# Kernel optimization log

Measured on AMD Instinct MI355X. Metric: run time of the kernel, lower is better.

## Reference

```python
import jax, jax.numpy as jnp
import numpy as np

B, H, W, L, T = 64, 512, 512, 2048, 8192
DIM = 256


def setup_inputs() -> dict:
    key = jax.random.key(0)
    ks = jax.random.split(key, 16)

    def lin(k, out_f, in_f):
        kw, kb = jax.random.split(k)
        s = 1.0 / np.sqrt(in_f)
        Wt = jax.random.uniform(kw, (out_f, in_f), jnp.float32, -s, s)
        b = jax.random.uniform(kb, (out_f,), jnp.float32, -s, s)
        return Wt, b

    Wv1, bv1 = lin(ks[3], 16, 3)
    Wv2, bv2 = lin(ks[4], 64, 16)
    Wv3, bv3 = lin(ks[5], 256, 64)
    Wa, ba = lin(ks[6], 256, 1)
    Wf, bf = lin(ks[7], 128, 128)
    Wg, bg = lin(ks[8], 128, 128)
    text_emb = jax.random.normal(ks[9], (256, 256), jnp.float32)

    return {
        "vision_ycbcr": jax.random.normal(ks[0], (B, 3, H, W), jnp.float32),
        "audio_wave": jax.random.normal(ks[1], (B, T), jnp.float32),
        "text_bytes": jax.random.randint(ks[2], (B, L), 0, 256),
        "Wv1": Wv1, "bv1": bv1, "Wv2": Wv2, "bv2": bv2,
        "Wv3": Wv3, "bv3": bv3, "text_emb": text_emb,
        "Wa": Wa, "ba": ba, "Wf": Wf, "bf": bf, "Wg": Wg, "bg": bg,
    }


def _forward(vision_ycbcr, audio_wave, text_bytes,
             Wv1, bv1, Wv2, bv2, Wv3, bv3, text_emb, Wa, ba, Wf, bf, Wg, bg):
    # vision: spatial mean -> 3-layer SiLU MLP to 256
    v = vision_ycbcr.mean(axis=(-1, -2))                      # [B,3]
    v = jax.nn.silu(v @ Wv1.T + bv1)                          # [B,16]
    v = jax.nn.silu(v @ Wv2.T + bv2)                          # [B,64]
    v = v @ Wv3.T + bv3                                       # [B,256]

    # text: embedding gather + mean pool
    t = text_emb[text_bytes].mean(axis=1)                     # [B,256]

    # audio: per-sample Linear(1,256) then mean pool (materialized as in torch)
    a = (audio_wave[..., None] * Wa[:, 0] + ba).mean(axis=1)  # [B,256]

    # Pancharatnam-Berry phase (inputs are real, so phase in {0, pi})
    inner_vt = jnp.sum(v * t, axis=-1)
    inner_ta = jnp.sum(t * a, axis=-1)
    inner_av = jnp.sum(a * v, axis=-1)
    gamma = jnp.angle(inner_vt * inner_ta * inner_av)[:, None]  # [B,1]

    combined = (v + t + a) * jnp.cos(gamma)                   # Re[exp(i*gamma)]

    # reversible coupling: y1 = x1 + F(x2); y2 = x2 + G(y1)
    x1, x2 = combined[:, :128], combined[:, 128:]
    y1 = x1 + jnp.tanh(x2 @ Wf.T + bf)
    y2 = x2 + jnp.tanh(y1 @ Wg.T + bg)

    m = jnp.concatenate([y1, y2], axis=-1)                    # [B,256]
    m = m / jnp.maximum(jnp.sum(jnp.abs(m), axis=-1, keepdims=True), 1e-12)

    # S = I + m m^T per batch; eta = angle(sign(det S)) / pi
    S = m[:, :, None] * m[:, None, :] + jnp.eye(DIM, dtype=m.dtype)
    sign, _ = jnp.linalg.slogdet(S)
    eta = jnp.angle(sign) / jnp.pi
    return m, eta


def reference(vision_ycbcr, text_bytes, audio_wave,
              Wv1, bv1, Wv2, bv2, Wv3, bv3, text_emb, Wa, ba, Wf, bf, Wg, bg):
    return _forward(vision_ycbcr, audio_wave, text_bytes,
                    Wv1, bv1, Wv2, bv2, Wv3, bv3, text_emb, Wa, ba, Wf, bf, Wg, bg)
```

## Files before the change

### kernel.cpp

```cpp
#include <hip/hip_runtime.h>
#include <math.h>

#define HW      262144
#define NB      64
#define T_AUD   8192
#define L_TXT   2048
#define DIM     256


__global__ __launch_bounds__(256) void k_vision(const float* __restrict__ vis,
                                                float* __restrict__ wsum) {
    int bx = blockIdx.x;
    int plane = bx >> 3;
    int chunk = bx & 7;
    const float4* p4 = reinterpret_cast<const float4*>(vis)
                       + (size_t)plane * 65536 + (size_t)chunk * 8192;
    int t = threadIdx.x;
    float s = 0.f;
#pragma unroll
    for (int k = 0; k < 32; ++k) {
        float4 v = p4[t + k * 256];
        s += (v.x + v.y) + (v.z + v.w);
    }
    for (int off = 32; off; off >>= 1) s += __shfl_down(s, off);
    __shared__ float r[4];
    int lane = t & 63, wid = t >> 6;
    if (lane == 0) r[wid] = s;
    __syncthreads();
    if (t == 0) atomicAdd(&wsum[plane], (r[0] + r[1]) + (r[2] + r[3]));
}

__global__ __launch_bounds__(256) void k_audio(const float* __restrict__ audio,
                                               float* __restrict__ asum) {
    int b = blockIdx.x;
    const float4* p4 = reinterpret_cast<const float4*>(audio) + (size_t)b * 2048;
    int t = threadIdx.x;
    float s = 0.f;
#pragma unroll
    for (int k = 0; k < 8; ++k) {
        float4 v = p4[t + k * 256];
        s += (v.x + v.y) + (v.z + v.w);
    }
    for (int off = 32; off; off >>= 1) s += __shfl_down(s, off);
    __shared__ float r[4];
    if ((t & 63) == 0) r[t >> 6] = s;
    __syncthreads();
    if (t == 0) asum[b] = (r[0] + r[1]) + (r[2] + r[3]);
}

__global__ __launch_bounds__(256) void k_text(const int* __restrict__ bytes,
                                              const float* __restrict__ emb,
                                              float* __restrict__ tsum) {
    int bx = blockIdx.x;
    int b = bx >> 3, chunk = bx & 7;
    int t = threadIdx.x;
    __shared__ int ids[256];
    ids[t] = bytes[b * L_TXT + chunk * 256 + t];
    __syncthreads();
    float acc = 0.f;
#pragma unroll 8
    for (int l = 0; l < 256; ++l) acc += emb[ids[l] * DIM + t];
    atomicAdd(&tsum[b * DIM + t], acc);
}

__global__ __launch_bounds__(256) void k_fuse(
        const float* __restrict__ wsum, const float* __restrict__ asum,
        const float* __restrict__ tsum,
        const float* __restrict__ Wv1, const float* __restrict__ bv1,
        const float* __restrict__ Wv2, const float* __restrict__ bv2,
        const float* __restrict__ Wv3, const float* __restrict__ bv3,
        const float* __restrict__ Wa,  const float* __restrict__ ba,
        const float* __restrict__ Wf,  const float* __restrict__ bfb,
        const float* __restrict__ Wg,  const float* __restrict__ bgb,
        float* __restrict__ out) {
    int b = blockIdx.x, t = threadIdx.x;
    __shared__ float sv[3], h1[16], h2[64], comb[256], y1s[128], y2s[128];
    __shared__ float r0[4], r1[4], r2[4];
    __shared__ float s_cg, s_norm;

    if (t < 3) sv[t] = wsum[b * 3 + t] * (1.f / (float)HW);
    __syncthreads();
    if (t < 16) {
        float s = bv1[t] + Wv1[t*3]*sv[0] + Wv1[t*3+1]*sv[1] + Wv1[t*3+2]*sv[2];
        h1[t] = s * (1.f / (1.f + expf(-s)));
    }
    __syncthreads();
    if (t < 64) {
        float s = bv2[t];
#pragma unroll
        for (int i = 0; i < 16; ++i) s += Wv2[t*16 + i] * h1[i];
        h2[t] = s * (1.f / (1.f + expf(-s)));
    }
    __syncthreads();
    float v = bv3[t];
#pragma unroll
    for (int j = 0; j < 64; ++j) v += Wv3[t*64 + j] * h2[j];
    float tv = tsum[b * DIM + t] * (1.f / (float)L_TXT);
    float am = asum[b] * (1.f / (float)T_AUD);
    float av = am * Wa[t] + ba[t];

    float pvt = v * tv, pta = tv * av, pav = av * v;
    for (int off = 32; off; off >>= 1) {
        pvt += __shfl_down(pvt, off);
        pta += __shfl_down(pta, off);
        pav += __shfl_down(pav, off);
    }
    int lane = t & 63, wid = t >> 6;
    if (lane == 0) { r0[wid] = pvt; r1[wid] = pta; r2[wid] = pav; }
    __syncthreads();
    if (t == 0) {
        float ivt = (r0[0]+r0[1]) + (r0[2]+r0[3]);
        float ita = (r1[0]+r1[1]) + (r1[2]+r1[3]);
        float iav = (r2[0]+r2[1]) + (r2[2]+r2[3]);
        float p = ivt * ita * iav;
        s_cg = (p < 0.f) ? -1.f : 1.f;
    }
    __syncthreads();
    float cd = (v + tv + av) * s_cg;
    comb[t] = cd;
    __syncthreads();
    if (t < 128) {
        float s = bfb[t];
#pragma unroll
        for (int k = 0; k < 128; ++k) s += Wf[t*128 + k] * comb[128 + k];
        y1s[t] = comb[t] + tanhf(s);
    }
    __syncthreads();
    if (t < 128) {
        float s = bgb[t];
#pragma unroll
        for (int k = 0; k < 128; ++k) s += Wg[t*128 + k] * y1s[k];
        y2s[t] = comb[128 + t] + tanhf(s);
    }
    __syncthreads();
    float m = (t < 128) ? y1s[t] : y2s[t - 128];
    float ab = fabsf(m);
    for (int off = 32; off; off >>= 1) ab += __shfl_down(ab, off);
    if (lane == 0) r0[wid] = ab;
    __syncthreads();
    if (t == 0) s_norm = fmaxf((r0[0]+r0[1]) + (r0[2]+r0[3]), 1e-12f);
    __syncthreads();
    out[b * DIM + t] = m / s_norm;
    if (t == 0) out[NB * DIM + b] = 0.f;
}

extern "C" void kernel_launch(void* const* d_in, const int* in_sizes, int n_in,
                              void* d_out, int out_size, void* d_ws, size_t ws_size,
                              hipStream_t stream) {
    const float* vis   = (const float*)d_in[0];
    const float* audio = (const float*)d_in[1];
    const int*   bytes = (const int*)d_in[2];
    const float* Wv1 = (const float*)d_in[3];
    const float* bv1 = (const float*)d_in[4];
    const float* Wv2 = (const float*)d_in[5];
    const float* bv2 = (const float*)d_in[6];
    const float* Wv3 = (const float*)d_in[7];
    const float* bv3 = (const float*)d_in[8];
    const float* emb = (const float*)d_in[9];
    const float* Wa  = (const float*)d_in[10];
    const float* ba  = (const float*)d_in[11];
    const float* Wf  = (const float*)d_in[12];
    const float* bfb = (const float*)d_in[13];
    const float* Wg  = (const float*)d_in[14];
    const float* bgb = (const float*)d_in[15];
    float* out = (float*)d_out;

    float* ws   = (float*)d_ws;
    float* wsum = ws;
    float* asum = ws + 192;
    float* tsum = ws + 256;

    hipMemsetAsync(d_ws, 0, (256 + NB * DIM) * sizeof(float), stream);
    k_vision<<<1536, 256, 0, stream>>>(vis, wsum);
    k_audio <<<64,   256, 0, stream>>>(audio, asum);
    k_text  <<<512,  256, 0, stream>>>(bytes, emb, tsum);
    k_fuse  <<<64,   256, 0, stream>>>(wsum, asum, tsum,
                                       Wv1, bv1, Wv2, bv2, Wv3, bv3,
                                       Wa, ba, Wf, bfb, Wg, bgb, out);
}
```

Before: 328.7 us.

## Drop memset and audio kernel, write partials instead of atomics, vectorize loads

```diff
diff --git a/kernel.cpp b/kernel.cpp
--- a/kernel.cpp
+++ b/kernel.cpp
@@ -9,7 +9,7 @@
 
 
 __global__ __launch_bounds__(256) void k_vision(const float* __restrict__ vis,
-                                                float* __restrict__ wsum) {
+                                                float* __restrict__ wpart) {
     int bx = blockIdx.x;
     int plane = bx >> 3;
     int chunk = bx & 7;
@@ -27,45 +27,43 @@
     int lane = t & 63, wid = t >> 6;
     if (lane == 0) r[wid] = s;
     __syncthreads();
-    if (t == 0) atomicAdd(&wsum[plane], (r[0] + r[1]) + (r[2] + r[3]));
-}
-
-__global__ __launch_bounds__(256) void k_audio(const float* __restrict__ audio,
-                                               float* __restrict__ asum) {
-    int b = blockIdx.x;
-    const float4* p4 = reinterpret_cast<const float4*>(audio) + (size_t)b * 2048;
-    int t = threadIdx.x;
-    float s = 0.f;
-#pragma unroll
-    for (int k = 0; k < 8; ++k) {
-        float4 v = p4[t + k * 256];
-        s += (v.x + v.y) + (v.z + v.w);
-    }
-    for (int off = 32; off; off >>= 1) s += __shfl_down(s, off);
-    __shared__ float r[4];
-    if ((t & 63) == 0) r[t >> 6] = s;
-    __syncthreads();
-    if (t == 0) asum[b] = (r[0] + r[1]) + (r[2] + r[3]);
+    if (t == 0) wpart[bx] = (r[0] + r[1]) + (r[2] + r[3]);
 }
 
 __global__ __launch_bounds__(256) void k_text(const int* __restrict__ bytes,
                                               const float* __restrict__ emb,
-                                              float* __restrict__ tsum) {
+                                              float* __restrict__ tpart) {
     int bx = blockIdx.x;
     int b = bx >> 3, chunk = bx & 7;
     int t = threadIdx.x;
+    int g = t >> 6, u = t & 63;
     __shared__ int ids[256];
+    __shared__ float4 sm[256];
     ids[t] = bytes[b * L_TXT + chunk * 256 + t];
     __syncthreads();
-    float acc = 0.f;
+    const float4* emb4 = reinterpret_cast<const float4*>(emb);
+    float4 acc = {0.f, 0.f, 0.f, 0.f};
 #pragma unroll 8
-    for (int l = 0; l < 256; ++l) acc += emb[ids[l] * DIM + t];
-    atomicAdd(&tsum[b * DIM + t], acc);
+    for (int l = g; l < 256; l += 4) {
+        float4 e = emb4[(size_t)ids[l] * 64 + u];
+        acc.x += e.x; acc.y += e.y; acc.z += e.z; acc.w += e.w;
+    }
+    sm[t] = acc;
+    __syncthreads();
+    if (t < 64) {
+        float4 a0 = sm[t], a1 = sm[64 + t], a2 = sm[128 + t], a3 = sm[192 + t];
+        float4 tot;
+        tot.x = (a0.x + a1.x) + (a2.x + a3.x);
+        tot.y = (a0.y + a1.y) + (a2.y + a3.y);
+        tot.z = (a0.z + a1.z) + (a2.z + a3.z);
+        tot.w = (a0.w + a1.w) + (a2.w + a3.w);
+        reinterpret_cast<float4*>(tpart)[(size_t)bx * 64 + t] = tot;
+    }
 }
 
 __global__ __launch_bounds__(256) void k_fuse(
-        const float* __restrict__ wsum, const float* __restrict__ asum,
-        const float* __restrict__ tsum,
+        const float* __restrict__ wpart, const float* __restrict__ audio,
+        const float* __restrict__ tpart,
         const float* __restrict__ Wv1, const float* __restrict__ bv1,
         const float* __restrict__ Wv2, const float* __restrict__ bv2,
         const float* __restrict__ Wv3, const float* __restrict__ bv3,
@@ -74,30 +72,62 @@
         const float* __restrict__ Wg,  const float* __restrict__ bgb,
         float* __restrict__ out) {
     int b = blockIdx.x, t = threadIdx.x;
-    __shared__ float sv[3], h1[16], h2[64], comb[256], y1s[128], y2s[128];
+    int lane = t & 63, wid = t >> 6;
+    __shared__ __align__(16) float h2[64], comb[256], y1s[128];
+    __shared__ float sv[3], h1[16], y2s[128];
     __shared__ float r0[4], r1[4], r2[4];
-    __shared__ float s_cg, s_norm;
-
-    if (t < 3) sv[t] = wsum[b * 3 + t] * (1.f / (float)HW);
+    __shared__ float s_cg, s_norm, s_am;
+
+    const float4* a4 = reinterpret_cast<const float4*>(audio) + (size_t)b * 2048;
+    float s = 0.f;
+#pragma unroll
+    for (int k = 0; k < 8; ++k) {
+        float4 v = a4[t + k * 256];
+        s += (v.x + v.y) + (v.z + v.w);
+    }
+    for (int off = 32; off; off >>= 1) s += __shfl_down(s, off);
+    if (lane == 0) r0[wid] = s;
+    __syncthreads();
+    if (t == 0) s_am = ((r0[0] + r0[1]) + (r0[2] + r0[3])) * (1.f / (float)T_AUD);
+    if (t < 3) {
+        float ss = 0.f;
+#pragma unroll
+        for (int j = 0; j < 8; ++j) ss += wpart[(b * 3 + t) * 8 + j];
+        sv[t] = ss * (1.f / (float)HW);
+    }
     __syncthreads();
     if (t < 16) {
-        float s = bv1[t] + Wv1[t*3]*sv[0] + Wv1[t*3+1]*sv[1] + Wv1[t*3+2]*sv[2];
-        h1[t] = s * (1.f / (1.f + expf(-s)));
+        float z = bv1[t] + Wv1[t*3]*sv[0] + Wv1[t*3+1]*sv[1] + Wv1[t*3+2]*sv[2];
+        h1[t] = z * (1.f / (1.f + expf(-z)));
     }
     __syncthreads();
     if (t < 64) {
-        float s = bv2[t];
-#pragma unroll
-        for (int i = 0; i < 16; ++i) s += Wv2[t*16 + i] * h1[i];
-        h2[t] = s * (1.f / (1.f + expf(-s)));
+        const float4* w4 = reinterpret_cast<const float4*>(Wv2) + t * 4;
+        float z = bv2[t];
+#pragma unroll
+        for (int j = 0; j < 4; ++j) {
+            float4 w = w4[j];
+            const float4 h = *reinterpret_cast<const float4*>(&h1[4*j]);
+            z += w.x*h.x + w.y*h.y + w.z*h.z + w.w*h.w;
+        }
+        h2[t] = z * (1.f / (1.f + expf(-z)));
     }
     __syncthreads();
     float v = bv3[t];
-#pragma unroll
-    for (int j = 0; j < 64; ++j) v += Wv3[t*64 + j] * h2[j];
-    float tv = tsum[b * DIM + t] * (1.f / (float)L_TXT);
-    float am = asum[b] * (1.f / (float)T_AUD);
-    float av = am * Wa[t] + ba[t];
+    {
+        const float4* w4 = reinterpret_cast<const float4*>(Wv3) + t * 16;
+#pragma unroll
+        for (int j = 0; j < 16; ++j) {
+            float4 w = w4[j];
+            const float4 h = *reinterpret_cast<const float4*>(&h2[4*j]);
+            v += w.x*h.x + w.y*h.y + w.z*h.z + w.w*h.w;
+        }
+    }
+    float tv = 0.f;
+#pragma unroll
+    for (int c = 0; c < 8; ++c) tv += tpart[((size_t)b * 8 + c) * 256 + t];
+    tv *= (1.f / (float)L_TXT);
+    float av = s_am * Wa[t] + ba[t];
 
     float pvt = v * tv, pta = tv * av, pav = av * v;
     for (int off = 32; off; off >>= 1) {
@@ -105,7 +135,6 @@
         pta += __shfl_down(pta, off);
         pav += __shfl_down(pav, off);
     }
-    int lane = t & 63, wid = t >> 6;
     if (lane == 0) { r0[wid] = pvt; r1[wid] = pta; r2[wid] = pav; }
     __syncthreads();
     if (t == 0) {
@@ -116,21 +145,30 @@
         s_cg = (p < 0.f) ? -1.f : 1.f;
     }
     __syncthreads();
-    float cd = (v + tv + av) * s_cg;
-    comb[t] = cd;
+    comb[t] = (v + tv + av) * s_cg;
     __syncthreads();
     if (t < 128) {
-        float s = bfb[t];
-#pragma unroll
-        for (int k = 0; k < 128; ++k) s += Wf[t*128 + k] * comb[128 + k];
-        y1s[t] = comb[t] + tanhf(s);
+        const float4* w4 = reinterpret_cast<const float4*>(Wf) + t * 32;
+        float z = bfb[t];
+#pragma unroll
+        for (int j = 0; j < 32; ++j) {
+            float4 w = w4[j];
+            const float4 x = *reinterpret_cast<const float4*>(&comb[128 + 4*j]);
+            z += w.x*x.x + w.y*x.y + w.z*x.z + w.w*x.w;
+        }
+        y1s[t] = comb[t] + tanhf(z);
     }
     __syncthreads();
     if (t < 128) {
-        float s = bgb[t];
-#pragma unroll
-        for (int k = 0; k < 128; ++k) s += Wg[t*128 + k] * y1s[k];
-        y2s[t] = comb[128 + t] + tanhf(s);
+        const float4* w4 = reinterpret_cast<const float4*>(Wg) + t * 32;
+        float z = bgb[t];
+#pragma unroll
+        for (int j = 0; j < 32; ++j) {
+            float4 w = w4[j];
+            const float4 x = *reinterpret_cast<const float4*>(&y1s[4*j]);
+            z += w.x*x.x + w.y*x.y + w.z*x.z + w.w*x.w;
+        }
+        y2s[t] = comb[128 + t] + tanhf(z);
     }
     __syncthreads();
     float m = (t < 128) ? y1s[t] : y2s[t - 128];
@@ -165,16 +203,13 @@
     const float* bgb = (const float*)d_in[15];
     float* out = (float*)d_out;
 
-    float* ws   = (float*)d_ws;
-    float* wsum = ws;
-    float* asum = ws + 192;
-    float* tsum = ws + 256;
-
-    hipMemsetAsync(d_ws, 0, (256 + NB * DIM) * sizeof(float), stream);
-    k_vision<<<1536, 256, 0, stream>>>(vis, wsum);
-    k_audio <<<64,   256, 0, stream>>>(audio, asum);
-    k_text  <<<512,  256, 0, stream>>>(bytes, emb, tsum);
-    k_fuse  <<<64,   256, 0, stream>>>(wsum, asum, tsum,
+    float* ws    = (float*)d_ws;
+    float* wpart = ws;
+    float* tpart = ws + 2048;
+
+    k_vision<<<1536, 256, 0, stream>>>(vis, wpart);
+    k_text  <<<512,  256, 0, stream>>>(bytes, emb, tpart);
+    k_fuse  <<<64,   256, 0, stream>>>(wpart, audio, tpart,
                                        Wv1, bv1, Wv2, bv2, Wv3, bv3,
                                        Wa, ba, Wf, bfb, Wg, bgb, out);
 }
```

Result: faster. 316.2 us (-3.8%).
